# Performance work log

Hardware: AMD Instinct MI355X
Metric: run time of the kernel (lower is better)

## Reference

```python
import jax, jax.numpy as jnp
import numpy as np

DEGREES = (0, 1, 2, 3)
REPEATS = np.array([2 * l + 1 for l in DEGREES])          # [1,3,5,7]
EV_DIM = int(REPEATS.sum())                               # 16
SEG = np.concatenate([[0], np.cumsum(REPEATS)])
F, H, L = 128, 8, len(DEGREES)
DH, DE = F // H, F // L                                   # 16, 32
NRB, N, E = 32, 16384, 262144
ATT_NORM_INV = float(np.sqrt(DH))
ATT_NORM_EV = float(np.sqrt(DE))


def l0_contraction(ev):
    # per-degree sum of squares over the m components: [..., EV_DIM] -> [..., L]
    return jnp.stack([jnp.sum(ev[..., SEG[i]:SEG[i + 1]] ** 2, axis=-1) for i in range(L)], axis=-1)


def silu(x):
    return x * jax.nn.sigmoid(x)


def filter_net(rbf, ev_inv, w1r, b1r, w2r, b2r, w1e, b1e, w2e, b2e):
    # FilterNet(num_layers=2): Linear+SiLU then Linear+Identity on each branch, summed.
    r = silu(rbf @ w1r + b1r) @ w2r + b2r
    e = silu(ev_inv @ w1e + b1e) @ w2e + b2e
    return r + e


def setup_inputs() -> dict:
    key = jax.random.key(0)
    ks = iter(jax.random.split(key, 40))
    nrm = lambda shape, s=1.0: jax.random.normal(next(ks), shape, dtype=jnp.float32) * s
    s = 0.05
    inp = {
        'inv_features': nrm((N, F)),
        'ev_features': nrm((N, EV_DIM)),
        'rbf': jax.random.uniform(next(ks), (E, NRB), dtype=jnp.float32),
        'sh_vectors': nrm((E, EV_DIM)),
        'cutoffs': jax.random.uniform(next(ks), (E, 1), dtype=jnp.float32),
        'senders': jax.random.randint(next(ks), (E,), 0, N),
        'receivers': jax.random.randint(next(ks), (E,), 0, N),
    }
    for p in ('fi', 'fe'):
        inp[p + '_rbf_w1'] = nrm((NRB, F), s); inp[p + '_rbf_b1'] = jnp.zeros((F,), jnp.float32)
        inp[p + '_rbf_w2'] = nrm((F, F), s);   inp[p + '_rbf_b2'] = jnp.zeros((F,), jnp.float32)
        inp[p + '_ev_w1'] = nrm((L, F // 4), s); inp[p + '_ev_b1'] = jnp.zeros((F // 4,), jnp.float32)
        inp[p + '_ev_w2'] = nrm((F // 4, F), s); inp[p + '_ev_b2'] = jnp.zeros((F,), jnp.float32)
    inp['Wq_inv'] = nrm((H, DH, DH), s)
    inp['Wk_inv'] = nrm((H, DH, DH), s)
    inp['Wv_inv'] = nrm((H, DH, DH), s)
    inp['Wq_ev'] = nrm((L, DE, DE), s)
    inp['Wk_ev'] = nrm((L, DE, DE), s)
    inp['int_w'] = nrm((F + L, F + L), s)
    inp['int_b'] = jnp.zeros((F + L,), jnp.float32)
    return inp


def reference(inv_features, ev_features, rbf, sh_vectors, cutoffs,
              fi_rbf_w1, fi_rbf_b1, fi_rbf_w2, fi_rbf_b2, fi_ev_w1, fi_ev_b1, fi_ev_w2, fi_ev_b2,
              fe_rbf_w1, fe_rbf_b1, fe_rbf_w2, fe_rbf_b2, fe_ev_w1, fe_ev_b1, fe_ev_w2, fe_ev_b2,
              Wq_inv, Wk_inv, Wv_inv, Wq_ev, Wk_ev, int_w, int_b,
              senders, receivers):
    n_nodes = inv_features.shape[0]
    # --- EuclideanAttentionBlock ---
    ev_diff = ev_features[senders] - ev_features[receivers]           # [E, EV_DIM]
    ev_diff_inv = l0_contraction(ev_diff)                             # [E, L]
    fw_inv = filter_net(rbf, ev_diff_inv, fi_rbf_w1, fi_rbf_b1, fi_rbf_w2, fi_rbf_b2,
                        fi_ev_w1, fi_ev_b1, fi_ev_w2, fi_ev_b2).reshape(-1, H, DH)
    fw_ev = filter_net(rbf, ev_diff_inv, fe_rbf_w1, fe_rbf_b1, fe_rbf_w2, fe_rbf_b2,
                       fe_ev_w1, fe_ev_b1, fe_ev_w2, fe_ev_b2).reshape(-1, L, DE)
    x_inv = inv_features.reshape(-1, H, DH)
    x_ev = inv_features.reshape(-1, L, DE)
    # qk_non_linearity = identity (None default)
    q_inv = jnp.einsum('nhd,hde->nhe', x_inv, Wq_inv)[receivers]      # [E, H, DH]
    k_inv = jnp.einsum('nhd,hde->nhe', x_inv, Wk_inv)[senders]
    v_inv = jnp.einsum('nhd,hde->nhe', x_inv, Wv_inv)[senders]
    q_ev = jnp.einsum('nld,lde->nle', x_ev, Wq_ev)[receivers]         # [E, L, DE]
    k_ev = jnp.einsum('nld,lde->nle', x_ev, Wk_ev)[senders]
    alpha_inv = jnp.sum(q_inv * (k_inv * fw_inv), axis=-1, keepdims=True) / ATT_NORM_INV  # [E,H,1]
    alpha_ev = jnp.sum(q_ev * (k_ev * fw_ev), axis=-1) / ATT_NORM_EV                      # [E,L]
    scaled_inv = cutoffs[:, :, None] * alpha_inv * v_inv              # [E, H, DH]
    d_att_inv = jax.ops.segment_sum(scaled_inv, receivers, num_segments=n_nodes).reshape(-1, F)
    alpha_ev_full = jnp.repeat(alpha_ev, REPEATS, axis=-1, total_repeat_length=EV_DIM)    # [E, EV_DIM]
    scaled_ev = cutoffs * alpha_ev_full * sh_vectors
    d_att_ev = jax.ops.segment_sum(scaled_ev, receivers, num_segments=n_nodes)
    inv1 = inv_features + d_att_inv
    ev1 = ev_features + d_att_ev
    # --- InteractionBlock ---
    ev_inv = l0_contraction(ev1)                                      # [N, L]
    t = jnp.concatenate([inv1, ev_inv], axis=-1) @ int_w + int_b      # [N, F+L]
    d_inv2 = t[..., :F]
    b_ev = jnp.repeat(t[..., F:], REPEATS, axis=-1, total_repeat_length=EV_DIM)
    d_ev2 = b_ev * ev1
    return inv1 + d_inv2, ev1 + d_ev2
```

## Files before the change

### kernel.cpp

```cpp
#include <hip/hip_runtime.h>
#include <math.h>

#define NN 16384
#define NRB 32
#define EE 262144
#define TEB 64
#define TPB_E 8
#define NPB_P 4

typedef __attribute__((ext_vector_type(8))) short short8v;
typedef __attribute__((ext_vector_type(4))) float f32x4;

__device__ __forceinline__ float silu_f(float x) {
    return x * __builtin_amdgcn_rcpf(1.0f + __expf(-x));
}
__device__ __forceinline__ int degmap(int j) { return (j == 0) ? 0 : (j < 4) ? 1 : (j < 9) ? 2 : 3; }
__device__ __forceinline__ unsigned short f2b(float f) {
    unsigned int u = __float_as_uint(f);
    unsigned int r = (u + 0x7FFFu + ((u >> 16) & 1u)) >> 16;
    return (unsigned short)r;
}
__device__ __forceinline__ float b2f(short s) {
    return __uint_as_float(((unsigned int)(unsigned short)s) << 16);
}

__global__ __launch_bounds__(256) void prep_weights(
    const float* __restrict__ fi_w1r, const float* __restrict__ fi_w2r,
    const float* __restrict__ fi_w2e,
    const float* __restrict__ fe_w1r, const float* __restrict__ fe_w2r,
    const float* __restrict__ fe_w2e,
    unsigned short* __restrict__ wbf)
{
    const int id = blockIdx.x * 256 + threadIdx.x;
    if (id >= 2 * 24576) return;
    const int p = id / 24576;
    const int r = id % 24576;
    const float* w1r = p ? fe_w1r : fi_w1r;
    const float* w2r = p ? fe_w2r : fi_w2r;
    const float* w2e = p ? fe_w2e : fi_w2e;
    float v;
    if (r < 4096) {
        v = w1r[(r & 31) * 128 + (r >> 5)];
    } else if (r < 20480) {
        const int rr = r - 4096;
        v = w2r[(rr & 127) * 128 + (rr >> 7)];
    } else {
        const int rr = r - 20480;
        v = w2e[(rr & 31) * 128 + (rr >> 5)];
    }
    wbf[p * 24576 + r] = f2b(v);
}

__global__ __launch_bounds__(128) void node_proj(
    const float* __restrict__ inv,
    const float* __restrict__ Wq_inv, const float* __restrict__ Wk_inv,
    const float* __restrict__ Wv_inv,
    const float* __restrict__ Wq_ev, const float* __restrict__ Wk_ev,
    unsigned short* __restrict__ q_inv, unsigned short* __restrict__ k_inv,
    unsigned short* __restrict__ v_inv,
    unsigned short* __restrict__ q_ev, unsigned short* __restrict__ k_ev)
{
    const int t = threadIdx.x;
    const int h = t >> 4, e = t & 15;
    const int l = t >> 5, e2 = t & 31;

    float wq[16], wk[16], wv[16];
    #pragma unroll
    for (int d = 0; d < 16; ++d) {
        wq[d] = Wq_inv[h * 256 + d * 16 + e];
        wk[d] = Wk_inv[h * 256 + d * 16 + e];
        wv[d] = Wv_inv[h * 256 + d * 16 + e];
    }
    float wqe[32], wke[32];
    #pragma unroll
    for (int d = 0; d < 32; ++d) {
        wqe[d] = Wq_ev[l * 1024 + d * 32 + e2];
        wke[d] = Wk_ev[l * 1024 + d * 32 + e2];
    }

    __shared__ float x[128];
    for (int nn = 0; nn < NPB_P; ++nn) {
        const int n = blockIdx.x * NPB_P + nn;
        __syncthreads();
        x[t] = inv[(size_t)n * 128 + t];
        __syncthreads();
        float aq = 0.f, ak = 0.f, av = 0.f;
        #pragma unroll
        for (int d = 0; d < 16; ++d) {
            const float xv = x[h * 16 + d];
            aq += xv * wq[d]; ak += xv * wk[d]; av += xv * wv[d];
        }
        q_inv[(size_t)n * 128 + t] = f2b(aq);
        k_inv[(size_t)n * 128 + t] = f2b(ak);
        v_inv[(size_t)n * 128 + t] = f2b(av);
        float bq = 0.f, bk = 0.f;
        #pragma unroll
        for (int d = 0; d < 32; ++d) {
            const float xv = x[l * 32 + d];
            bq += xv * wqe[d]; bk += xv * wke[d];
        }
        q_ev[(size_t)n * 128 + t] = f2b(bq);
        k_ev[(size_t)n * 128 + t] = f2b(bk);
    }
}

__global__ __launch_bounds__(256) void csr_count(const int* __restrict__ recv,
                                                 int* __restrict__ cnt) {
    const int e = blockIdx.x * 256 + threadIdx.x;
    if (e < EE) atomicAdd(&cnt[recv[e]], 1);
}

__global__ __launch_bounds__(256) void csr_scan(const int* __restrict__ cnt,
                                                int* __restrict__ off) {
    __shared__ int ps[256];
    const int t = threadIdx.x;
    const int base = t * 64;
    int s = 0;
    for (int i = 0; i < 64; ++i) s += cnt[base + i];
    ps[t] = s;
    __syncthreads();
    for (int dd = 1; dd < 256; dd <<= 1) {
        int v = 0;
        if (t >= dd) v = ps[t - dd];
        __syncthreads();
        ps[t] += v;
        __syncthreads();
    }
    int run = ps[t] - s;
    for (int i = 0; i < 64; ++i) {
        off[base + i] = run;
        run += cnt[base + i];
    }
}

__global__ __launch_bounds__(256) void csr_fill(const int* __restrict__ recv,
                                                const int* __restrict__ send,
                                                const float* __restrict__ rbf,
                                                const float* __restrict__ cutoffs,
                                                const int* __restrict__ off,
                                                int* __restrict__ cursor,
                                                int* __restrict__ s_eid,
                                                int* __restrict__ s_sid,
                                                int* __restrict__ s_rid,
                                                unsigned short* __restrict__ rbf_s,
                                                float* __restrict__ cut_s) {
    const int e = blockIdx.x * 256 + threadIdx.x;
    if (e < EE) {
        const int r = recv[e];
        const int p = off[r] + atomicAdd(&cursor[r], 1);
        s_eid[p] = e;
        s_sid[p] = send[e];
        s_rid[p] = r;
        cut_s[p] = cutoffs[e];
        const float* src = rbf + (size_t)e * 32;
        unsigned short* dst = rbf_s + (size_t)p * 32;
        #pragma unroll
        for (int c = 0; c < 4; ++c) {
            const float4 a = *(const float4*)(src + c * 8);
            const float4 b = *(const float4*)(src + c * 8 + 4);
            short8v pk;
            pk[0] = f2b(a.x); pk[1] = f2b(a.y); pk[2] = f2b(a.z); pk[3] = f2b(a.w);
            pk[4] = f2b(b.x); pk[5] = f2b(b.y); pk[6] = f2b(b.z); pk[7] = f2b(b.w);
            *(short8v*)(dst + c * 8) = pk;
        }
    }
}

__global__ __launch_bounds__(256) void edge_kernel(
    const float* __restrict__ ev_feat,
    const unsigned short* __restrict__ rbf_s,
    const float* __restrict__ cut_s,
    const int* __restrict__ s_sid,
    const int* __restrict__ s_rid,
    const unsigned short* __restrict__ wbf,
    const float* __restrict__ fi_b1r, const float* __restrict__ fi_b2r,
    const float* __restrict__ fi_w1e, const float* __restrict__ fi_b1e,
    const float* __restrict__ fi_b2e,
    const float* __restrict__ fe_b1r, const float* __restrict__ fe_b2r,
    const float* __restrict__ fe_w1e, const float* __restrict__ fe_b1e,
    const float* __restrict__ fe_b2e,
    const unsigned short* __restrict__ q_inv, const unsigned short* __restrict__ k_inv,
    const unsigned short* __restrict__ q_ev, const unsigned short* __restrict__ k_ev,
    float* __restrict__ alpha_g)
{
    __shared__ unsigned short w2lds[16384];
    __shared__ unsigned short rbuf[TEB][40];
    __shared__ unsigned short h1buf[TEB][136];
    __shared__ unsigned short hebuf[TEB][40];
    __shared__ float evinv_t[TEB][4];

    const int tid = threadIdx.x;
    const int lane = tid & 63;
    const int wv = tid >> 6;
    const int wb = wv * 16;
    const int e0 = blockIdx.x * (TEB * TPB_E);
    const int pass = blockIdx.y;
    const int lrow = lane & 15;
    const int lk = lane >> 4;
    const int rj = (lane & 3) * 8;
    const int rrow = lane >> 2;

    const unsigned short* w1rT = wbf + pass * 24576;
    const unsigned short* w2eT = w1rT + 20480;
    const float* b1r = pass ? fe_b1r : fi_b1r;
    const float* b2r = pass ? fe_b2r : fi_b2r;
    const float* w1e = pass ? fe_w1e : fi_w1e;
    const float* b1e = pass ? fe_b1e : fi_b1e;
    const float* b2e = pass ? fe_b2e : fi_b2e;
    const unsigned short* qtab = pass == 0 ? q_inv : q_ev;
    const unsigned short* ktab = pass == 0 ? k_inv : k_ev;

    {
        const short8v* src = (const short8v*)(wbf + pass * 24576 + 4096);
        short8v* dst = (short8v*)w2lds;
        #pragma unroll
        for (int i = 0; i < 8; ++i) {
            const int c = tid + 256 * i;
            const int col = c >> 4;
            const int slot = c & 15;
            dst[(c & ~15) | (slot ^ (col & 7))] = src[c];
        }
    }

    int sC, rC;
    float cC;
    short8v rbC;
    {
        const int ge = e0 + wb + lrow;
        sC = s_sid[ge]; rC = s_rid[ge]; cC = cut_s[ge];
        rbC = *(const short8v*)(rbf_s + (size_t)(e0 + wb + rrow) * 32 + rj);
    }
    __syncthreads();

    #pragma unroll 1
    for (int t = 0; t < TPB_E; ++t) {
        const int tbase = e0 + t * TEB;

        const unsigned short* qb = qtab + (size_t)rC * 128 + lk * 32;
        const unsigned short* kb = ktab + (size_t)sC * 128 + lk * 32;
        const short8v pq0 = *(const short8v*)qb;
        const short8v pq1 = *(const short8v*)(qb + 8);
        const short8v pq2 = *(const short8v*)(qb + 16);
        const short8v pq3 = *(const short8v*)(qb + 24);
        const short8v pk0 = *(const short8v*)kb;
        const short8v pk1 = *(const short8v*)(kb + 8);
        const short8v pk2 = *(const short8v*)(kb + 16);
        const short8v pk3 = *(const short8v*)(kb + 24);

        float4 es0, es1, es2, es3, er0, er1, er2, er3;
        if (lane < 16) {
            const float* es = ev_feat + (size_t)sC * 16;
            const float* er = ev_feat + (size_t)rC * 16;
            es0 = *(const float4*)es;       er0 = *(const float4*)er;
            es1 = *(const float4*)(es + 4); er1 = *(const float4*)(er + 4);
            es2 = *(const float4*)(es + 8); er2 = *(const float4*)(er + 8);
            es3 = *(const float4*)(es + 12); er3 = *(const float4*)(er + 12);
        }

        int sN = 0, rN = 0;
        float cN = 0.f;
        short8v rbN;
        if (t + 1 < TPB_E) {
            const int gn = tbase + TEB + wb + lrow;
            sN = s_sid[gn]; rN = s_rid[gn]; cN = cut_s[gn];
            rbN = *(const short8v*)(rbf_s + (size_t)(tbase + TEB + wb + rrow) * 32 + rj);
        }

        *(short8v*)&rbuf[wb + rrow][rj] = rbC;

        if (lane < 16) {
            float d0 = es0.x - er0.x;
            evinv_t[wb + lane][0] = d0 * d0;
            float a1 = (es0.y - er0.y) * (es0.y - er0.y)
                     + (es0.z - er0.z) * (es0.z - er0.z)
                     + (es0.w - er0.w) * (es0.w - er0.w);
            evinv_t[wb + lane][1] = a1;
            float a2 = (es1.x - er1.x) * (es1.x - er1.x)
                     + (es1.y - er1.y) * (es1.y - er1.y)
                     + (es1.z - er1.z) * (es1.z - er1.z)
                     + (es1.w - er1.w) * (es1.w - er1.w)
                     + (es2.x - er2.x) * (es2.x - er2.x);
            evinv_t[wb + lane][2] = a2;
            float a3 = (es2.y - er2.y) * (es2.y - er2.y)
                     + (es2.z - er2.z) * (es2.z - er2.z)
                     + (es2.w - er2.w) * (es2.w - er2.w)
                     + (es3.x - er3.x) * (es3.x - er3.x)
                     + (es3.y - er3.y) * (es3.y - er3.y)
                     + (es3.z - er3.z) * (es3.z - er3.z)
                     + (es3.w - er3.w) * (es3.w - er3.w);
            evinv_t[wb + lane][3] = a3;
        }

        {
            const short8v a1 = *(const short8v*)&rbuf[wb + lrow][lk * 8];
            #pragma unroll
            for (int tt = 0; tt < 8; ++tt) {
                const int col = tt * 16 + lrow;
                const float b = b1r[col];
                f32x4 c; c[0] = b; c[1] = b; c[2] = b; c[3] = b;
                const short8v bv = *(const short8v*)(w1rT + (size_t)col * 32 + lk * 8);
                c = __builtin_amdgcn_mfma_f32_16x16x32_bf16(a1, bv, c, 0, 0, 0);
                #pragma unroll
                for (int rg = 0; rg < 4; ++rg)
                    h1buf[wb + lk * 4 + rg][col] = f2b(silu_f(c[rg]));
            }
        }
        {
            const int le = wb + rrow;
            const float v0 = evinv_t[le][0], v1 = evinv_t[le][1];
            const float v2 = evinv_t[le][2], v3 = evinv_t[le][3];
            short8v pk_;
            #pragma unroll
            for (int q = 0; q < 2; ++q) {
                const int j = rj + q * 4;
                const float4 bb = *(const float4*)(b1e + j);
                const float4 r0 = *(const float4*)(w1e + j);
                const float4 r1 = *(const float4*)(w1e + 32 + j);
                const float4 r2 = *(const float4*)(w1e + 64 + j);
                const float4 r3 = *(const float4*)(w1e + 96 + j);
                pk_[q * 4 + 0] = f2b(silu_f(bb.x + v0 * r0.x + v1 * r1.x + v2 * r2.x + v3 * r3.x));
                pk_[q * 4 + 1] = f2b(silu_f(bb.y + v0 * r0.y + v1 * r1.y + v2 * r2.y + v3 * r3.y));
                pk_[q * 4 + 2] = f2b(silu_f(bb.z + v0 * r0.z + v1 * r1.z + v2 * r2.z + v3 * r3.z));
                pk_[q * 4 + 3] = f2b(silu_f(bb.w + v0 * r0.w + v1 * r1.w + v2 * r2.w + v3 * r3.w));
            }
            *(short8v*)&hebuf[le][rj] = pk_;
        }

        f32x4 acc[8];
        #pragma unroll
        for (int tt = 0; tt < 8; ++tt) {
            const int col = tt * 16 + lrow;
            const float b = b2r[col] + b2e[col];
            acc[tt][0] = b; acc[tt][1] = b; acc[tt][2] = b; acc[tt][3] = b;
        }
        #pragma unroll
        for (int ks = 0; ks < 4; ++ks) {
            const short8v av = *(const short8v*)&h1buf[wb + lrow][ks * 32 + lk * 8];
            const int slot = ks * 4 + lk;
            #pragma unroll
            for (int tt = 0; tt < 8; ++tt) {
                const int col = tt * 16 + lrow;
                const short8v bv = *(const short8v*)&w2lds[
                    col * 128 + ((slot ^ (lrow & 7)) << 3)];
                acc[tt] = __builtin_amdgcn_mfma_f32_16x16x32_bf16(av, bv, acc[tt], 0, 0, 0);
            }
        }
        {
            const short8v ae = *(const short8v*)&hebuf[wb + lrow][lk * 8];
            #pragma unroll
            for (int tt = 0; tt < 8; ++tt) {
                const short8v bv = *(const short8v*)(
                    w2eT + (size_t)(tt * 16 + lrow) * 32 + lk * 8);
                acc[tt] = __builtin_amdgcn_mfma_f32_16x16x32_bf16(ae, bv, acc[tt], 0, 0, 0);
            }
        }
        #pragma unroll
        for (int tt = 0; tt < 8; ++tt) {
            const int col = tt * 16 + lrow;
            #pragma unroll
            for (int rg = 0; rg < 4; ++rg)
                h1buf[wb + lk * 4 + rg][col] = f2b(acc[tt][rg]);
        }

        const int slot = tbase + wb + lrow;
        if (pass == 0) {
            const int le = wb + lrow;
            #pragma unroll
            for (int it = 0; it < 2; ++it) {
                const int h = lk * 2 + it;
                const short8v f0 = *(const short8v*)&h1buf[le][h * 16];
                const short8v f1 = *(const short8v*)&h1buf[le][h * 16 + 8];
                const short8v qa = it ? pq2 : pq0;
                const short8v qc = it ? pq3 : pq1;
                const short8v ka = it ? pk2 : pk0;
                const short8v kc = it ? pk3 : pk1;
                float dot = 0.f;
                #pragma unroll
                for (int j = 0; j < 8; ++j)
                    dot += b2f(qa[j]) * b2f(ka[j]) * b2f(f0[j]);
                #pragma unroll
                for (int j = 0; j < 8; ++j)
                    dot += b2f(qc[j]) * b2f(kc[j]) * b2f(f1[j]);
                alpha_g[(size_t)slot * 12 + h] = dot * 0.25f * cC;
            }
        } else {
            const int le = wb + lrow;
            const int l = lk;
            float dot = 0.f;
            #pragma unroll
            for (int c8 = 0; c8 < 4; ++c8) {
                const short8v fv = *(const short8v*)&h1buf[le][l * 32 + c8 * 8];
                const short8v qv = (c8 == 0) ? pq0 : (c8 == 1) ? pq1 : (c8 == 2) ? pq2 : pq3;
                const short8v kv = (c8 == 0) ? pk0 : (c8 == 1) ? pk1 : (c8 == 2) ? pk2 : pk3;
                #pragma unroll
                for (int j = 0; j < 8; ++j)
                    dot += b2f(qv[j]) * b2f(kv[j]) * b2f(fv[j]);
            }
            alpha_g[(size_t)slot * 12 + 8 + l] = dot * 0.17677669529663687f * cC;
        }

        sC = sN; rC = rN; cC = cN; rbC = rbN;
    }
}

__global__ __launch_bounds__(256) void node_update(
    const float* __restrict__ inv, const float* __restrict__ ev,
    const unsigned short* __restrict__ v_inv, const float* __restrict__ sh,
    const float* __restrict__ alpha_g,
    const int* __restrict__ cnt, const int* __restrict__ off,
    const int* __restrict__ s_eid, const int* __restrict__ s_sid,
    const float* __restrict__ int_w, const float* __restrict__ int_b,
    float* __restrict__ out0, float* __restrict__ out1)
{
    const int tid = threadIdx.x;
    const int g16 = tid >> 4;
    const int fl16 = tid & 15;
    const int f16 = fl16 * 8;
    const int hsel = f16 >> 4;
    const int n = blockIdx.x;
    const int d = cnt[n];
    const int o = off[n];

    float accv[8];
    #pragma unroll
    for (int j = 0; j < 8; ++j) accv[j] = 0.f;
    float acce = 0.f;
    const int esel = 8 + degmap(fl16);

    for (int i = g16; i < d; i += 16) {
        const int p = o + i;
        const int sid = s_sid[p];
        const float a = alpha_g[(size_t)p * 12 + hsel];
        const short8v v = *(const short8v*)(v_inv + (size_t)sid * 128 + f16);
        #pragma unroll
        for (int j = 0; j < 8; ++j) accv[j] += a * b2f(v[j]);
        const int eid = s_eid[p];
        acce += alpha_g[(size_t)p * 12 + esel] * sh[(size_t)eid * 16 + fl16];
    }

    __shared__ float pv[16][128];
    __shared__ float pe[16][16];
    __shared__ float xin[132];
    __shared__ float ev1s[16];
    __shared__ float tcol[4];

    #pragma unroll
    for (int j = 0; j < 8; ++j) pv[g16][f16 + j] = accv[j];
    pe[g16][fl16] = acce;
    __syncthreads();

    float iv = 0.f;
    if (tid < 128) {
        float s = 0.f;
        #pragma unroll
        for (int gg = 0; gg < 16; ++gg) s += pv[gg][tid];
        iv = inv[(size_t)n * 128 + tid] + s;
        xin[tid] = iv;
        if (tid < 16) {
            float se = 0.f;
            #pragma unroll
            for (int gg = 0; gg < 16; ++gg) se += pe[gg][tid];
            ev1s[tid] = ev[(size_t)n * 16 + tid] + se;
        }
    }
    __syncthreads();
    if (tid < 4) {
        const int st = (tid == 0) ? 0 : (tid == 1) ? 1 : (tid == 2) ? 4 : 9;
        const int en = (tid == 0) ? 1 : (tid == 1) ? 4 : (tid == 2) ? 9 : 16;
        float a = 0.f;
        for (int j = st; j < en; ++j) a += ev1s[j] * ev1s[j];
        xin[128 + tid] = a;
    }
    __syncthreads();

    const int g = tid >> 5;
    const int fl = tid & 31;
    const int f = fl * 4;
    float4 macc; macc.x = 0.f; macc.y = 0.f; macc.z = 0.f; macc.w = 0.f;
    float macc2 = 0.f;
    const int k0 = g * 17;
    const int k1 = (k0 + 17 < 132) ? k0 + 17 : 132;
    for (int k = k0; k < k1; ++k) {
        const float xv = xin[k];
        const float4 w4 = *(const float4*)(int_w + k * 132 + f);
        macc.x += xv * w4.x; macc.y += xv * w4.y;
        macc.z += xv * w4.z; macc.w += xv * w4.w;
        if (fl < 4) macc2 += xv * int_w[k * 132 + 128 + fl];
    }
    __syncthreads();
    *reinterpret_cast<float4*>(&pv[g][f]) = macc;
    if (fl < 4) pe[g][fl] = macc2;
    __syncthreads();

    if (tid < 128) {
        float s = int_b[tid];
        #pragma unroll
        for (int gg = 0; gg < 8; ++gg) s += pv[gg][tid];
        out0[(size_t)n * 128 + tid] = iv + s;
        if (tid < 4) {
            float s2 = int_b[128 + tid];
            #pragma unroll
            for (int gg = 0; gg < 8; ++gg) s2 += pe[gg][tid];
            tcol[tid] = s2;
        }
    }
    __syncthreads();
    if (tid < 16) out1[(size_t)n * 16 + tid] = ev1s[tid] * (1.0f + tcol[degmap(tid)]);
}

extern "C" void kernel_launch(void* const* d_in, const int* in_sizes, int n_in,
                              void* d_out, int out_size, void* d_ws, size_t ws_size,
                              hipStream_t stream) {
    const float* inv_features = (const float*)d_in[0];
    const float* ev_features  = (const float*)d_in[1];
    const float* rbf          = (const float*)d_in[2];
    const float* sh_vectors   = (const float*)d_in[3];
    const float* cutoffs      = (const float*)d_in[4];
    const int*   senders      = (const int*)d_in[5];
    const int*   receivers    = (const int*)d_in[6];
    const float* fi_rbf_w1 = (const float*)d_in[7];
    const float* fi_rbf_b1 = (const float*)d_in[8];
    const float* fi_rbf_w2 = (const float*)d_in[9];
    const float* fi_rbf_b2 = (const float*)d_in[10];
    const float* fi_ev_w1  = (const float*)d_in[11];
    const float* fi_ev_b1  = (const float*)d_in[12];
    const float* fi_ev_w2  = (const float*)d_in[13];
    const float* fi_ev_b2  = (const float*)d_in[14];
    const float* fe_rbf_w1 = (const float*)d_in[15];
    const float* fe_rbf_b1 = (const float*)d_in[16];
    const float* fe_rbf_w2 = (const float*)d_in[17];
    const float* fe_rbf_b2 = (const float*)d_in[18];
    const float* fe_ev_w1  = (const float*)d_in[19];
    const float* fe_ev_b1  = (const float*)d_in[20];
    const float* fe_ev_w2  = (const float*)d_in[21];
    const float* fe_ev_b2  = (const float*)d_in[22];
    const float* Wq_inv = (const float*)d_in[23];
    const float* Wk_inv = (const float*)d_in[24];
    const float* Wv_inv = (const float*)d_in[25];
    const float* Wq_ev  = (const float*)d_in[26];
    const float* Wk_ev  = (const float*)d_in[27];
    const float* int_w  = (const float*)d_in[28];
    const float* int_b  = (const float*)d_in[29];

    float* ws = (float*)d_ws;
    unsigned short* q_inv = (unsigned short*)ws;
    unsigned short* k_inv = q_inv + (size_t)NN * 128;
    unsigned short* v_inv = q_inv + (size_t)NN * 256;
    unsigned short* q_ev  = q_inv + (size_t)NN * 384;
    unsigned short* k_ev  = q_inv + (size_t)NN * 512;
    float* alpha_g = ws + (size_t)NN * 320;
    int*   cnt     = (int*)(ws + (size_t)NN * 512);
    int*   off     = cnt + NN;
    int*   cursor  = cnt + 2 * NN;
    int*   s_eid   = cnt + 3 * NN;
    int*   s_sid   = s_eid + EE;
    int*   s_rid   = s_sid + EE;
    float* cut_s   = (float*)(s_rid + EE);
    unsigned short* rbf_s = (unsigned short*)(cut_s + EE);
    unsigned short* wbf = rbf_s + (size_t)EE * 32;

    hipMemsetAsync(cnt, 0, (size_t)3 * NN * sizeof(int), stream);

    prep_weights<<<192, 256, 0, stream>>>(fi_rbf_w1, fi_rbf_w2, fi_ev_w2,
                                          fe_rbf_w1, fe_rbf_w2, fe_ev_w2, wbf);

    node_proj<<<NN / NPB_P, 128, 0, stream>>>(inv_features, Wq_inv, Wk_inv, Wv_inv,
                                              Wq_ev, Wk_ev, q_inv, k_inv, v_inv, q_ev, k_ev);

    csr_count<<<EE / 256, 256, 0, stream>>>(receivers, cnt);
    csr_scan<<<1, 256, 0, stream>>>(cnt, off);
    csr_fill<<<EE / 256, 256, 0, stream>>>(receivers, senders, rbf, cutoffs, off, cursor,
                                           s_eid, s_sid, s_rid, rbf_s, cut_s);

    dim3 egrid(EE / (TEB * TPB_E), 2);
    edge_kernel<<<egrid, 256, 0, stream>>>(
        ev_features, rbf_s, cut_s, s_sid, s_rid, wbf,
        fi_rbf_b1, fi_rbf_b2, fi_ev_w1, fi_ev_b1, fi_ev_b2,
        fe_rbf_b1, fe_rbf_b2, fe_ev_w1, fe_ev_b1, fe_ev_b2,
        q_inv, k_inv, q_ev, k_ev, alpha_g);

    node_update<<<NN, 256, 0, stream>>>(inv_features, ev_features, v_inv, sh_vectors,
                                        alpha_g, cnt, off, s_eid, s_sid,
                                        int_w, int_b,
                                        (float*)d_out, (float*)d_out + (size_t)NN * 128);
}
```

Baseline: 272.4 us.

## Fuse the two filter-net passes into one edge kernel launch

The edge kernel previously ran as a 2-wide grid in y, with one pass for the invariant filter and one for the equivariant filter, and each pass reloaded the edge metadata, rbf tile and ev features. Now a single block computes both filters per edge tile, sharing the loaded indices, rbf rows and ev-difference invariants, and keeps both W2 matrices in LDS. This halves the grid and removes the duplicated gathers and the second prologue. In exchange it doubles LDS usage to about 64KB for weights plus buffers, which likely lowers occupancy, and it raises register pressure because the q/k vectors of both passes are live at once.

```diff
diff --git a/kernel.cpp b/kernel.cpp
--- a/kernel.cpp
+++ b/kernel.cpp
@@ -183,7 +183,7 @@
     const unsigned short* __restrict__ q_ev, const unsigned short* __restrict__ k_ev,
     float* __restrict__ alpha_g)
 {
-    __shared__ unsigned short w2lds[16384];
+    __shared__ unsigned short w2lds[32768];
     __shared__ unsigned short rbuf[TEB][40];
     __shared__ unsigned short h1buf[TEB][136];
     __shared__ unsigned short hebuf[TEB][40];
@@ -194,31 +194,28 @@
     const int wv = tid >> 6;
     const int wb = wv * 16;
     const int e0 = blockIdx.x * (TEB * TPB_E);
-    const int pass = blockIdx.y;
     const int lrow = lane & 15;
     const int lk = lane >> 4;
     const int rj = (lane & 3) * 8;
     const int rrow = lane >> 2;
 
-    const unsigned short* w1rT = wbf + pass * 24576;
-    const unsigned short* w2eT = w1rT + 20480;
-    const float* b1r = pass ? fe_b1r : fi_b1r;
-    const float* b2r = pass ? fe_b2r : fi_b2r;
-    const float* w1e = pass ? fe_w1e : fi_w1e;
-    const float* b1e = pass ? fe_b1e : fi_b1e;
-    const float* b2e = pass ? fe_b2e : fi_b2e;
-    const unsigned short* qtab = pass == 0 ? q_inv : q_ev;
-    const unsigned short* ktab = pass == 0 ? k_inv : k_ev;
+    const unsigned short* w1rT_i = wbf;
+    const unsigned short* w2eT_i = wbf + 20480;
+    const unsigned short* w1rT_e = wbf + 24576;
+    const unsigned short* w2eT_e = wbf + 24576 + 20480;
 
     {
-        const short8v* src = (const short8v*)(wbf + pass * 24576 + 4096);
+        const short8v* src0 = (const short8v*)(wbf + 4096);
+        const short8v* src1 = (const short8v*)(wbf + 24576 + 4096);
         short8v* dst = (short8v*)w2lds;
         #pragma unroll
         for (int i = 0; i < 8; ++i) {
             const int c = tid + 256 * i;
             const int col = c >> 4;
             const int slot = c & 15;
-            dst[(c & ~15) | (slot ^ (col & 7))] = src[c];
+            const int d = (c & ~15) | (slot ^ (col & 7));
+            dst[d] = src0[c];
+            dst[2048 + d] = src1[c];
         }
     }
 
@@ -235,9 +232,11 @@
     #pragma unroll 1
     for (int t = 0; t < TPB_E; ++t) {
         const int tbase = e0 + t * TEB;
-
-        const unsigned short* qb = qtab + (size_t)rC * 128 + lk * 32;
-        const unsigned short* kb = ktab + (size_t)sC * 128 + lk * 32;
+        const int le = wb + lrow;
+        const int slot12 = tbase + wb + lrow;
+
+        const unsigned short* qb = q_inv + (size_t)rC * 128 + lk * 32;
+        const unsigned short* kb = k_inv + (size_t)sC * 128 + lk * 32;
         const short8v pq0 = *(const short8v*)qb;
         const short8v pq1 = *(const short8v*)(qb + 8);
         const short8v pq2 = *(const short8v*)(qb + 16);
@@ -296,107 +295,190 @@
             #pragma unroll
             for (int tt = 0; tt < 8; ++tt) {
                 const int col = tt * 16 + lrow;
-                const float b = b1r[col];
+                const float b = fi_b1r[col];
                 f32x4 c; c[0] = b; c[1] = b; c[2] = b; c[3] = b;
-                const short8v bv = *(const short8v*)(w1rT + (size_t)col * 32 + lk * 8);
+                const short8v bv = *(const short8v*)(w1rT_i + (size_t)col * 32 + lk * 8);
                 c = __builtin_amdgcn_mfma_f32_16x16x32_bf16(a1, bv, c, 0, 0, 0);
                 #pragma unroll
                 for (int rg = 0; rg < 4; ++rg)
                     h1buf[wb + lk * 4 + rg][col] = f2b(silu_f(c[rg]));
             }
         }
+        const unsigned short* qeb = q_ev + (size_t)rC * 128 + lk * 32;
+        const unsigned short* keb = k_ev + (size_t)sC * 128 + lk * 32;
+        const short8v pqe0 = *(const short8v*)qeb;
+        const short8v pqe1 = *(const short8v*)(qeb + 8);
+        const short8v pqe2 = *(const short8v*)(qeb + 16);
+        const short8v pqe3 = *(const short8v*)(qeb + 24);
+        const short8v pke0 = *(const short8v*)keb;
+        const short8v pke1 = *(const short8v*)(keb + 8);
+        const short8v pke2 = *(const short8v*)(keb + 16);
+        const short8v pke3 = *(const short8v*)(keb + 24);
+
         {
-            const int le = wb + rrow;
-            const float v0 = evinv_t[le][0], v1 = evinv_t[le][1];
-            const float v2 = evinv_t[le][2], v3 = evinv_t[le][3];
+            const int lee = wb + rrow;
+            const float v0 = evinv_t[lee][0], v1 = evinv_t[lee][1];
+            const float v2 = evinv_t[lee][2], v3 = evinv_t[lee][3];
             short8v pk_;
             #pragma unroll
             for (int q = 0; q < 2; ++q) {
                 const int j = rj + q * 4;
-                const float4 bb = *(const float4*)(b1e + j);
-                const float4 r0 = *(const float4*)(w1e + j);
-                const float4 r1 = *(const float4*)(w1e + 32 + j);
-                const float4 r2 = *(const float4*)(w1e + 64 + j);
-                const float4 r3 = *(const float4*)(w1e + 96 + j);
+                const float4 bb = *(const float4*)(fi_b1e + j);
+                const float4 r0 = *(const float4*)(fi_w1e + j);
+                const float4 r1 = *(const float4*)(fi_w1e + 32 + j);
+                const float4 r2 = *(const float4*)(fi_w1e + 64 + j);
+                const float4 r3 = *(const float4*)(fi_w1e + 96 + j);
                 pk_[q * 4 + 0] = f2b(silu_f(bb.x + v0 * r0.x + v1 * r1.x + v2 * r2.x + v3 * r3.x));
                 pk_[q * 4 + 1] = f2b(silu_f(bb.y + v0 * r0.y + v1 * r1.y + v2 * r2.y + v3 * r3.y));
                 pk_[q * 4 + 2] = f2b(silu_f(bb.z + v0 * r0.z + v1 * r1.z + v2 * r2.z + v3 * r3.z));
                 pk_[q * 4 + 3] = f2b(silu_f(bb.w + v0 * r0.w + v1 * r1.w + v2 * r2.w + v3 * r3.w));
             }
-            *(short8v*)&hebuf[le][rj] = pk_;
-        }
-
-        f32x4 acc[8];
-        #pragma unroll
-        for (int tt = 0; tt < 8; ++tt) {
-            const int col = tt * 16 + lrow;
-            const float b = b2r[col] + b2e[col];
-            acc[tt][0] = b; acc[tt][1] = b; acc[tt][2] = b; acc[tt][3] = b;
-        }
-        #pragma unroll
-        for (int ks = 0; ks < 4; ++ks) {
-            const short8v av = *(const short8v*)&h1buf[wb + lrow][ks * 32 + lk * 8];
-            const int slot = ks * 4 + lk;
+            *(short8v*)&hebuf[lee][rj] = pk_;
+        }
+
+        {
+            f32x4 acc[8];
             #pragma unroll
             for (int tt = 0; tt < 8; ++tt) {
                 const int col = tt * 16 + lrow;
-                const short8v bv = *(const short8v*)&w2lds[
-                    col * 128 + ((slot ^ (lrow & 7)) << 3)];
-                acc[tt] = __builtin_amdgcn_mfma_f32_16x16x32_bf16(av, bv, acc[tt], 0, 0, 0);
-            }
-        }
+                const float b = fi_b2r[col] + fi_b2e[col];
+                acc[tt][0] = b; acc[tt][1] = b; acc[tt][2] = b; acc[tt][3] = b;
+            }
+            #pragma unroll
+            for (int ks = 0; ks < 4; ++ks) {
+                const short8v av = *(const short8v*)&h1buf[wb + lrow][ks * 32 + lk * 8];
+                const int slot = ks * 4 + lk;
+                #pragma unroll
+                for (int tt = 0; tt < 8; ++tt) {
+                    const int col = tt * 16 + lrow;
+                    const short8v bv = *(const short8v*)&w2lds[
+                        col * 128 + ((slot ^ (lrow & 7)) << 3)];
+                    acc[tt] = __builtin_amdgcn_mfma_f32_16x16x32_bf16(av, bv, acc[tt], 0, 0, 0);
+                }
+            }
+            {
+                const short8v ae = *(const short8v*)&hebuf[wb + lrow][lk * 8];
+                #pragma unroll
+                for (int tt = 0; tt < 8; ++tt) {
+                    const short8v bv = *(const short8v*)(
+                        w2eT_i + (size_t)(tt * 16 + lrow) * 32 + lk * 8);
+                    acc[tt] = __builtin_amdgcn_mfma_f32_16x16x32_bf16(ae, bv, acc[tt], 0, 0, 0);
+                }
+            }
+            #pragma unroll
+            for (int tt = 0; tt < 8; ++tt) {
+                const int col = tt * 16 + lrow;
+                #pragma unroll
+                for (int rg = 0; rg < 4; ++rg)
+                    h1buf[wb + lk * 4 + rg][col] = f2b(acc[tt][rg]);
+            }
+        }
+
+        #pragma unroll
+        for (int it = 0; it < 2; ++it) {
+            const int h = lk * 2 + it;
+            const short8v f0 = *(const short8v*)&h1buf[le][h * 16];
+            const short8v f1 = *(const short8v*)&h1buf[le][h * 16 + 8];
+            const short8v qa = it ? pq2 : pq0;
+            const short8v qc = it ? pq3 : pq1;
+            const short8v ka = it ? pk2 : pk0;
+            const short8v kc = it ? pk3 : pk1;
+            float dot = 0.f;
+            #pragma unroll
+            for (int j = 0; j < 8; ++j)
+                dot += b2f(qa[j]) * b2f(ka[j]) * b2f(f0[j]);
+            #pragma unroll
+            for (int j = 0; j < 8; ++j)
+                dot += b2f(qc[j]) * b2f(kc[j]) * b2f(f1[j]);
+            alpha_g[(size_t)slot12 * 12 + h] = dot * 0.25f * cC;
+        }
+
         {
-            const short8v ae = *(const short8v*)&hebuf[wb + lrow][lk * 8];
+            const short8v a1 = *(const short8v*)&rbuf[wb + lrow][lk * 8];
             #pragma unroll
             for (int tt = 0; tt < 8; ++tt) {
-                const short8v bv = *(const short8v*)(
-                    w2eT + (size_t)(tt * 16 + lrow) * 32 + lk * 8);
-                acc[tt] = __builtin_amdgcn_mfma_f32_16x16x32_bf16(ae, bv, acc[tt], 0, 0, 0);
-            }
-        }
-        #pragma unroll
-        for (int tt = 0; tt < 8; ++tt) {
-            const int col = tt * 16 + lrow;
-            #pragma unroll
-            for (int rg = 0; rg < 4; ++rg)
-                h1buf[wb + lk * 4 + rg][col] = f2b(acc[tt][rg]);
-        }
-
-        const int slot = tbase + wb + lrow;
-        if (pass == 0) {
-            const int le = wb + lrow;
-            #pragma unroll
-            for (int it = 0; it < 2; ++it) {
-                const int h = lk * 2 + it;
-                const short8v f0 = *(const short8v*)&h1buf[le][h * 16];
-                const short8v f1 = *(const short8v*)&h1buf[le][h * 16 + 8];
-                const short8v qa = it ? pq2 : pq0;
-                const short8v qc = it ? pq3 : pq1;
-                const short8v ka = it ? pk2 : pk0;
-                const short8v kc = it ? pk3 : pk1;
-                float dot = 0.f;
-                #pragma unroll
-                for (int j = 0; j < 8; ++j)
-                    dot += b2f(qa[j]) * b2f(ka[j]) * b2f(f0[j]);
-                #pragma unroll
-                for (int j = 0; j < 8; ++j)
-                    dot += b2f(qc[j]) * b2f(kc[j]) * b2f(f1[j]);
-                alpha_g[(size_t)slot * 12 + h] = dot * 0.25f * cC;
-            }
-        } else {
-            const int le = wb + lrow;
+                const int col = tt * 16 + lrow;
+                const float b = fe_b1r[col];
+                f32x4 c; c[0] = b; c[1] = b; c[2] = b; c[3] = b;
+                const short8v bv = *(const short8v*)(w1rT_e + (size_t)col * 32 + lk * 8);
+                c = __builtin_amdgcn_mfma_f32_16x16x32_bf16(a1, bv, c, 0, 0, 0);
+                #pragma unroll
+                for (int rg = 0; rg < 4; ++rg)
+                    h1buf[wb + lk * 4 + rg][col] = f2b(silu_f(c[rg]));
+            }
+        }
+        {
+            const int lee = wb + rrow;
+            const float v0 = evinv_t[lee][0], v1 = evinv_t[lee][1];
+            const float v2 = evinv_t[lee][2], v3 = evinv_t[lee][3];
+            short8v pk_;
+            #pragma unroll
+            for (int q = 0; q < 2; ++q) {
+                const int j = rj + q * 4;
+                const float4 bb = *(const float4*)(fe_b1e + j);
+                const float4 r0 = *(const float4*)(fe_w1e + j);
+                const float4 r1 = *(const float4*)(fe_w1e + 32 + j);
+                const float4 r2 = *(const float4*)(fe_w1e + 64 + j);
+                const float4 r3 = *(const float4*)(fe_w1e + 96 + j);
+                pk_[q * 4 + 0] = f2b(silu_f(bb.x + v0 * r0.x + v1 * r1.x + v2 * r2.x + v3 * r3.x));
+                pk_[q * 4 + 1] = f2b(silu_f(bb.y + v0 * r0.y + v1 * r1.y + v2 * r2.y + v3 * r3.y));
+                pk_[q * 4 + 2] = f2b(silu_f(bb.z + v0 * r0.z + v1 * r1.z + v2 * r2.z + v3 * r3.z));
+                pk_[q * 4 + 3] = f2b(silu_f(bb.w + v0 * r0.w + v1 * r1.w + v2 * r2.w + v3 * r3.w));
+            }
+            *(short8v*)&hebuf[lee][rj] = pk_;
+        }
+
+        {
+            f32x4 acc[8];
+            #pragma unroll
+            for (int tt = 0; tt < 8; ++tt) {
+                const int col = tt * 16 + lrow;
+                const float b = fe_b2r[col] + fe_b2e[col];
+                acc[tt][0] = b; acc[tt][1] = b; acc[tt][2] = b; acc[tt][3] = b;
+            }
+            #pragma unroll
+            for (int ks = 0; ks < 4; ++ks) {
+                const short8v av = *(const short8v*)&h1buf[wb + lrow][ks * 32 + lk * 8];
+                const int slot = ks * 4 + lk;
+                #pragma unroll
+                for (int tt = 0; tt < 8; ++tt) {
+                    const int col = tt * 16 + lrow;
+                    const short8v bv = *(const short8v*)&w2lds[
+                        16384 + col * 128 + ((slot ^ (lrow & 7)) << 3)];
+                    acc[tt] = __builtin_amdgcn_mfma_f32_16x16x32_bf16(av, bv, acc[tt], 0, 0, 0);
+                }
+            }
+            {
+                const short8v ae = *(const short8v*)&hebuf[wb + lrow][lk * 8];
+                #pragma unroll
+                for (int tt = 0; tt < 8; ++tt) {
+                    const short8v bv = *(const short8v*)(
+                        w2eT_e + (size_t)(tt * 16 + lrow) * 32 + lk * 8);
+                    acc[tt] = __builtin_amdgcn_mfma_f32_16x16x32_bf16(ae, bv, acc[tt], 0, 0, 0);
+                }
+            }
+            #pragma unroll
+            for (int tt = 0; tt < 8; ++tt) {
+                const int col = tt * 16 + lrow;
+                #pragma unroll
+                for (int rg = 0; rg < 4; ++rg)
+                    h1buf[wb + lk * 4 + rg][col] = f2b(acc[tt][rg]);
+            }
+        }
+
+        {
             const int l = lk;
             float dot = 0.f;
             #pragma unroll
             for (int c8 = 0; c8 < 4; ++c8) {
                 const short8v fv = *(const short8v*)&h1buf[le][l * 32 + c8 * 8];
-                const short8v qv = (c8 == 0) ? pq0 : (c8 == 1) ? pq1 : (c8 == 2) ? pq2 : pq3;
-                const short8v kv = (c8 == 0) ? pk0 : (c8 == 1) ? pk1 : (c8 == 2) ? pk2 : pk3;
+                const short8v qv = (c8 == 0) ? pqe0 : (c8 == 1) ? pqe1 : (c8 == 2) ? pqe2 : pqe3;
+                const short8v kv = (c8 == 0) ? pke0 : (c8 == 1) ? pke1 : (c8 == 2) ? pke2 : pke3;
                 #pragma unroll
                 for (int j = 0; j < 8; ++j)
                     dot += b2f(qv[j]) * b2f(kv[j]) * b2f(fv[j]);
             }
-            alpha_g[(size_t)slot * 12 + 8 + l] = dot * 0.17677669529663687f * cC;
+            alpha_g[(size_t)slot12 * 12 + 8 + l] = dot * 0.17677669529663687f * cC;
         }
 
         sC = sN; rC = rN; cC = cN; rbC = rbN;
@@ -572,8 +654,7 @@
     csr_fill<<<EE / 256, 256, 0, stream>>>(receivers, senders, rbf, cutoffs, off, cursor,
                                            s_eid, s_sid, s_rid, rbf_s, cut_s);
 
-    dim3 egrid(EE / (TEB * TPB_E), 2);
-    edge_kernel<<<egrid, 256, 0, stream>>>(
+    edge_kernel<<<EE / (TEB * TPB_E), 256, 0, stream>>>(
         ev_features, rbf_s, cut_s, s_sid, s_rid, wbf,
         fi_rbf_b1, fi_rbf_b2, fi_ev_w1, fi_ev_b1, fi_ev_b2,
         fe_rbf_b1, fe_rbf_b2, fe_ev_w1, fe_ev_b1, fe_ev_b2,
```

After: 307.1 us. 1.13x slower.
